# Kernel optimization log

Hardware: AMD Instinct MI355X
Metric: run time of the kernel (lower is better)

The kernel has to match this reference:

```python
import jax, jax.numpy as jnp
import numpy as np

B, N, L = 64, 256, 1024
OUT = L // 2   # ChebConv out_channels = Seq_len / 2
ALPHA = 0.5    # DirGNNConv default alpha


def _glorot(key, shape):
    # PyG ChebConv lins use glorot init
    lim = float(np.sqrt(6.0 / (shape[0] + shape[1])))
    return jax.random.uniform(key, shape, minval=-lim, maxval=lim, dtype=jnp.float32)


def setup_inputs() -> dict:
    key = jax.random.key(0)
    ks = jax.random.split(key, 8)
    x = jax.random.normal(ks[0], (B, N, L), dtype=jnp.float32)
    # dense per-sample adjacency; only used via nonzero() in torch, never enters math (K=1)
    At = jax.random.randint(ks[1], (B, N, N), 0, 2, dtype=jnp.int32)
    W_in = _glorot(ks[2], (L, OUT))
    b_in = jnp.zeros((OUT,), dtype=jnp.float32)
    W_out = _glorot(ks[3], (L, OUT))
    b_out = jnp.zeros((OUT,), dtype=jnp.float32)
    # DirGNNConv root Linear (kaiming-ish uniform; exact init irrelevant for correctness baseline)
    lim = float(1.0 / np.sqrt(L))
    W_root = jax.random.uniform(ks[4], (L, OUT), minval=-lim, maxval=lim, dtype=jnp.float32)
    b_root = jax.random.uniform(ks[5], (OUT,), minval=-lim, maxval=lim, dtype=jnp.float32)
    return {"x": x, "At": At, "W_in": W_in, "b_in": b_in,
            "W_out": W_out, "b_out": b_out, "W_root": W_root, "b_root": b_root}


def reference(x, At, W_in, b_in, W_out, b_out, W_root, b_root):
    # so the batched edge_index built from At.nonzero() never influences the output.
    # DirGNNConv: alpha * conv_out(x) + (1-alpha) * conv_in(x) + root_lin(x).
    xf = x.reshape(B * N, L)                        # [B*N, L]
    y = (ALPHA * (xf @ W_out + b_out)
         + (1.0 - ALPHA) * (xf @ W_in + b_in)
         + (xf @ W_root + b_root))                  # [B*N, OUT]
    return y.reshape(B, N, OUT)
```

## Files before the change

kernel.cpp:

```cpp
#include <hip/hip_runtime.h>
#include <stdint.h>

static constexpr int Kdim  = 1024;
static constexpr int Ncols = 512;

typedef __attribute__((ext_vector_type(8))) short bf16x8;
typedef __attribute__((ext_vector_type(4))) float f32x4;

union pk8 { uint4 u; bf16x8 h; };

__device__ __forceinline__ unsigned short f2bf(float f) {
  unsigned u = __builtin_bit_cast(unsigned, f);
  u += 0x7FFFu + ((u >> 16) & 1u);
  return (unsigned short)(u >> 16);
}
__device__ __forceinline__ unsigned f2bf2(float lo, float hi) {
  unsigned ul = __builtin_bit_cast(unsigned, lo);
  unsigned uh = __builtin_bit_cast(unsigned, hi);
  ul += 0x7FFFu + ((ul >> 16) & 1u);
  uh += 0x7FFFu + ((uh >> 16) & 1u);
  return (ul >> 16) | (uh & 0xFFFF0000u);
}

__device__ __forceinline__ void gl2lds16(const void* g, void* l) {
  __builtin_amdgcn_global_load_lds(
      (const __attribute__((address_space(1))) void*)g,
      (__attribute__((address_space(3))) void*)l, 16, 0, 0);
}

__global__ __launch_bounds__(256) void combine_w(
    const float* __restrict__ Win, const float* __restrict__ Wout,
    const float* __restrict__ Wroot, unsigned short* __restrict__ Wt)
{
  __shared__ unsigned short lds[32 * 36];
  const int bid = blockIdx.x;
  const int tk0 = (bid & 31) * 32;
  const int tn0 = (bid >> 5) * 32;
  const int t = threadIdx.x;
  {
    const int k  = t >> 3;
    const int nq = (t & 7) * 4;
    const int gi = (tk0 + k) * Ncols + tn0 + nq;
    const float4 wi = *(const float4*)(Win + gi);
    const float4 wo = *(const float4*)(Wout + gi);
    const float4 wr = *(const float4*)(Wroot + gi);
    lds[(nq + 0) * 36 + k] = f2bf(0.5f * (wi.x + wo.x) + wr.x);
    lds[(nq + 1) * 36 + k] = f2bf(0.5f * (wi.y + wo.y) + wr.y);
    lds[(nq + 2) * 36 + k] = f2bf(0.5f * (wi.z + wo.z) + wr.z);
    lds[(nq + 3) * 36 + k] = f2bf(0.5f * (wi.w + wo.w) + wr.w);
  }
  __syncthreads();
  {
    const int n  = t >> 3;
    const int k8 = (t & 7) * 4;
    const ushort4 v = *(const ushort4*)&lds[n * 36 + k8];
    *(ushort4*)(Wt + (size_t)(tn0 + n) * Kdim + tk0 + k8) = v;
  }
}

__global__ __launch_bounds__(256, 4) void gemm_fused3(
    const float* __restrict__ X, const unsigned short* __restrict__ Wt,
    const float* __restrict__ b_in, const float* __restrict__ b_out,
    const float* __restrict__ b_root, float* __restrict__ Y)
{
  __shared__ __attribute__((aligned(16))) float As[2][64 * 32];
  __shared__ __attribute__((aligned(16))) short Bs[2][128 * 32];

  const int bid = blockIdx.x;
  const int m0 = (bid & 255) * 64;
  const int n0 = (bid >> 8) * 128;

  const int t    = threadIdx.x;
  const int lane = t & 63;
  const int w    = t >> 6;
  const int wm   = w >> 1;
  const int wn   = w & 1;
  const int quad = lane >> 4;
  const int lm   = lane & 15;

  const int ra = lane >> 3;
  const int sa = lane & 7;
  const int ca = sa ^ ra;
  const float* gA0 = X + (size_t)(m0 + w * 16 + ra) * Kdim + ca * 4;
  const float* gA1 = gA0 + (size_t)8 * Kdim;
  const int lA0 = (w * 16) * 32;
  const int lA1 = (w * 16 + 8) * 32;

  const int rb = lane >> 2;
  const int sb = lane & 3;
  const int cb = sb ^ ((rb ^ (rb >> 2)) & 3);
  const unsigned short* gB0 = Wt + (size_t)(n0 + w * 32 + rb) * Kdim + cb * 8;
  const unsigned short* gB1 = gB0 + (size_t)16 * Kdim;
  const int lB0 = (w * 32) * 32;
  const int lB1 = (w * 32 + 16) * 32;

  const int sA0 = (2 * quad) ^ (lm & 7);
  const int sA1 = sA0 ^ 1;
  const int aoff = (wm * 32 + lm) * 32;
  const int swzB = quad ^ ((lm ^ (lm >> 2)) & 3);
  const int boff = (wn * 64 + lm) * 32 + swzB * 8;

  f32x4 acc[2][4] = {};

  gl2lds16(gA0, &As[0][lA0]);
  gl2lds16(gA1, &As[0][lA1]);
  gl2lds16(gB0, &Bs[0][lB0]);
  gl2lds16(gB1, &Bs[0][lB1]);

  #pragma unroll 1
  for (int it = 0; it < 32; ++it) {
    const int p = it & 1;
    const int q = p ^ 1;
    __syncthreads();

    const int nx = (it < 31 ? it + 1 : 31) * 32;
    gl2lds16(gA0 + nx, &As[q][lA0]);
    gl2lds16(gA1 + nx, &As[q][lA1]);
    gl2lds16(gB0 + nx, &Bs[q][lB0]);
    gl2lds16(gB1 + nx, &Bs[q][lB1]);

    bf16x8 bfr[4];
    #pragma unroll
    for (int j = 0; j < 4; ++j)
      bfr[j] = *(const bf16x8*)&Bs[p][boff + j * 512];

    bf16x8 af[2];
    #pragma unroll
    for (int i = 0; i < 2; ++i) {
      const f32x4 lo = *(const f32x4*)&As[p][aoff + i * 512 + sA0 * 4];
      const f32x4 hi = *(const f32x4*)&As[p][aoff + i * 512 + sA1 * 4];
      pk8 pk;
      pk.u.x = f2bf2(lo.x, lo.y);
      pk.u.y = f2bf2(lo.z, lo.w);
      pk.u.z = f2bf2(hi.x, hi.y);
      pk.u.w = f2bf2(hi.z, hi.w);
      af[i] = pk.h;
    }

    #pragma unroll
    for (int i = 0; i < 2; ++i)
      #pragma unroll
      for (int j = 0; j < 4; ++j)
        acc[i][j] = __builtin_amdgcn_mfma_f32_16x16x32_bf16(af[i], bfr[j], acc[i][j], 0, 0, 0);
  }

  #pragma unroll
  for (int j = 0; j < 4; ++j) {
    const int gc = n0 + wn * 64 + j * 16 + lm;
    const float bias = 0.5f * (b_in[gc] + b_out[gc]) + b_root[gc];
    #pragma unroll
    for (int i = 0; i < 2; ++i) {
      const int gr = m0 + wm * 32 + i * 16 + quad * 4;
      float* yp = Y + (size_t)gr * Ncols + gc;
      #pragma unroll
      for (int r = 0; r < 4; ++r)
        yp[(size_t)r * Ncols] = acc[i][j][r] + bias;
    }
  }
}

extern "C" void kernel_launch(void* const* d_in, const int* in_sizes, int n_in,
                              void* d_out, int out_size, void* d_ws, size_t ws_size,
                              hipStream_t stream)
{
  const float* x      = (const float*)d_in[0];
  const float* W_in   = (const float*)d_in[2];
  const float* b_in   = (const float*)d_in[3];
  const float* W_out  = (const float*)d_in[4];
  const float* b_out  = (const float*)d_in[5];
  const float* W_root = (const float*)d_in[6];
  const float* b_root = (const float*)d_in[7];
  float* y = (float*)d_out;

  unsigned short* Wt = (unsigned short*)d_ws;

  combine_w <<<dim3(512),  dim3(256), 0, stream>>>(W_in, W_out, W_root, Wt);
  gemm_fused3<<<dim3(1024), dim3(256), 0, stream>>>(x, Wt, b_in, b_out, b_root, y);
}
```

Measured before the change: 160.3 us.

## Cover full N per block so X is read and converted once

The GEMM now uses 512-thread blocks that each compute a 64-row by full 512-column output tile, instead of 64x128 tiles across four column blocks. The goal is to stop reading X (fp32) from global memory four times and to do its bf16 conversion only once per block. In exchange the launch has just 256 blocks on a GPU with many CUs, which lowers occupancy and parallelism. It also raises LDS use for B, and each wave now converts the whole A tile redundantly.

```diff
diff --git a/kernel.cpp b/kernel.cpp
--- a/kernel.cpp
+++ b/kernel.cpp
@@ -58,77 +58,74 @@
   }
 }
 
-__global__ __launch_bounds__(256, 4) void gemm_fused3(
+__global__ __launch_bounds__(512, 2) void gemm_fullN(
     const float* __restrict__ X, const unsigned short* __restrict__ Wt,
     const float* __restrict__ b_in, const float* __restrict__ b_out,
     const float* __restrict__ b_root, float* __restrict__ Y)
 {
   __shared__ __attribute__((aligned(16))) float As[2][64 * 32];
-  __shared__ __attribute__((aligned(16))) short Bs[2][128 * 32];
+  __shared__ __attribute__((aligned(16))) short Bs[2][512 * 32];
 
-  const int bid = blockIdx.x;
-  const int m0 = (bid & 255) * 64;
-  const int n0 = (bid >> 8) * 128;
+  const int m0 = blockIdx.x * 64;
 
   const int t    = threadIdx.x;
   const int lane = t & 63;
   const int w    = t >> 6;
-  const int wm   = w >> 1;
-  const int wn   = w & 1;
   const int quad = lane >> 4;
   const int lm   = lane & 15;
 
   const int ra = lane >> 3;
-  const int sa = lane & 7;
-  const int ca = sa ^ ra;
-  const float* gA0 = X + (size_t)(m0 + w * 16 + ra) * Kdim + ca * 4;
-  const float* gA1 = gA0 + (size_t)8 * Kdim;
-  const int lA0 = (w * 16) * 32;
-  const int lA1 = (w * 16 + 8) * 32;
+  const int ca = (lane & 7) ^ ra;
+  const float* gA = X + (size_t)(m0 + w * 8 + ra) * Kdim + ca * 4;
+  float* const lA = &As[0][0] + (w * 8) * 32;
+  const int bufA = 64 * 32;
 
   const int rb = lane >> 2;
-  const int sb = lane & 3;
-  const int cb = sb ^ ((rb ^ (rb >> 2)) & 3);
-  const unsigned short* gB0 = Wt + (size_t)(n0 + w * 32 + rb) * Kdim + cb * 8;
-  const unsigned short* gB1 = gB0 + (size_t)16 * Kdim;
-  const int lB0 = (w * 32) * 32;
-  const int lB1 = (w * 32 + 16) * 32;
+  const int cb = (lane & 3) ^ ((rb >> 1) & 3);
+  const unsigned short* gB = Wt + (size_t)(w * 64 + rb) * Kdim + cb * 8;
+  short* const lB = &Bs[0][0] + (w * 64) * 32;
+  const int bufB = 512 * 32;
+  const int rowK16 = 16 * Kdim;
 
-  const int sA0 = (2 * quad) ^ (lm & 7);
-  const int sA1 = sA0 ^ 1;
-  const int aoff = (wm * 32 + lm) * 32;
-  const int swzB = quad ^ ((lm ^ (lm >> 2)) & 3);
-  const int boff = (wn * 64 + lm) * 32 + swzB * 8;
+  const int sA0   = (2 * quad) ^ (lm & 7);
+  const int slotB = quad ^ ((lm >> 1) & 3);
+  const int aoff  = lm * 32;
+  const int boff  = (w * 64 + lm) * 32 + slotB * 8;
 
-  f32x4 acc[2][4] = {};
+  f32x4 acc[4][4] = {};
 
-  gl2lds16(gA0, &As[0][lA0]);
-  gl2lds16(gA1, &As[0][lA1]);
-  gl2lds16(gB0, &Bs[0][lB0]);
-  gl2lds16(gB1, &Bs[0][lB1]);
+  gl2lds16(gA, lA);
+  #pragma unroll
+  for (int g = 0; g < 4; ++g)
+    gl2lds16(gB + (size_t)g * rowK16, lB + g * 512);
 
   #pragma unroll 1
   for (int it = 0; it < 32; ++it) {
-    const int p = it & 1;
+    const int p = (it & 1);
     const int q = p ^ 1;
     __syncthreads();
 
-    const int nx = (it < 31 ? it + 1 : 31) * 32;
-    gl2lds16(gA0 + nx, &As[q][lA0]);
-    gl2lds16(gA1 + nx, &As[q][lA1]);
-    gl2lds16(gB0 + nx, &Bs[q][lB0]);
-    gl2lds16(gB1 + nx, &Bs[q][lB1]);
+    if (it != 31) {
+      const int nx = (it + 1) * 32;
+      gl2lds16(gA + nx, lA + q * bufA);
+      #pragma unroll
+      for (int g = 0; g < 4; ++g)
+        gl2lds16(gB + nx + (size_t)g * rowK16, lB + q * bufB + g * 512);
+    }
+
+    const float* Ap = &As[0][0] + p * bufA;
+    const short* Bp = &Bs[0][0] + p * bufB;
 
     bf16x8 bfr[4];
     #pragma unroll
     for (int j = 0; j < 4; ++j)
-      bfr[j] = *(const bf16x8*)&Bs[p][boff + j * 512];
+      bfr[j] = *(const bf16x8*)&Bp[boff + j * 512];
 
-    bf16x8 af[2];
+    bf16x8 af[4];
     #pragma unroll
-    for (int i = 0; i < 2; ++i) {
-      const f32x4 lo = *(const f32x4*)&As[p][aoff + i * 512 + sA0 * 4];
-      const f32x4 hi = *(const f32x4*)&As[p][aoff + i * 512 + sA1 * 4];
+    for (int i = 0; i < 4; ++i) {
+      const f32x4 lo = *(const f32x4*)&Ap[i * 512 + aoff + sA0 * 4];
+      const f32x4 hi = *(const f32x4*)&Ap[i * 512 + aoff + (sA0 ^ 1) * 4];
       pk8 pk;
       pk.u.x = f2bf2(lo.x, lo.y);
       pk.u.y = f2bf2(lo.z, lo.w);
@@ -138,7 +135,7 @@
     }
 
     #pragma unroll
-    for (int i = 0; i < 2; ++i)
+    for (int i = 0; i < 4; ++i)
       #pragma unroll
       for (int j = 0; j < 4; ++j)
         acc[i][j] = __builtin_amdgcn_mfma_f32_16x16x32_bf16(af[i], bfr[j], acc[i][j], 0, 0, 0);
@@ -146,11 +143,11 @@
 
   #pragma unroll
   for (int j = 0; j < 4; ++j) {
-    const int gc = n0 + wn * 64 + j * 16 + lm;
+    const int gc = w * 64 + j * 16 + lm;
     const float bias = 0.5f * (b_in[gc] + b_out[gc]) + b_root[gc];
     #pragma unroll
-    for (int i = 0; i < 2; ++i) {
-      const int gr = m0 + wm * 32 + i * 16 + quad * 4;
+    for (int i = 0; i < 4; ++i) {
+      const int gr = m0 + i * 16 + quad * 4;
       float* yp = Y + (size_t)gr * Ncols + gc;
       #pragma unroll
       for (int r = 0; r < 4; ++r)
@@ -174,6 +171,6 @@
 
   unsigned short* Wt = (unsigned short*)d_ws;
 
-  combine_w <<<dim3(512),  dim3(256), 0, stream>>>(W_in, W_out, W_root, Wt);
-  gemm_fused3<<<dim3(1024), dim3(256), 0, stream>>>(x, Wt, b_in, b_out, b_root, y);
+  combine_w <<<dim3(512), dim3(256), 0, stream>>>(W_in, W_out, W_root, Wt);
+  gemm_fullN<<<dim3(256), dim3(512), 0, stream>>>(x, Wt, b_in, b_out, b_root, y);
 }
```

Result: slower. 165.7 us (+3.4%).
